# Kernel tuning notes

Measured on AMD Instinct MI355X. Metric: run time of the kernel, lower is better.

Reference implementation:

```python
import jax, jax.numpy as jnp
import numpy as np

# Fixed hyperparameters from init_kwargs
KH, KW = 3, 3
GRID_SIZE = 5
SPLINE_ORDER = 3
GRID_RANGE = (-1.0, 1.0)


def _make_grid():
    # grid buffer: arange(-k, grid_size + k + 1) * h + grid_range[0], shape (G + 2k + 1,) = (12,)
    h = (GRID_RANGE[1] - GRID_RANGE[0]) / GRID_SIZE
    return (jnp.arange(-SPLINE_ORDER, GRID_SIZE + SPLINE_ORDER + 1, dtype=jnp.float32) * h
            + GRID_RANGE[0])


def _unfold(x):
    # torch.nn.Unfold with kernel (3,3), stride 1, pad 0, dilation 1.
    # Returns (N, C*KH*KW) with channel-major ordering (c, i, j), matching torch.
    B, C, H, W = x.shape
    Ho, Wo = H - KH + 1, W - KW + 1
    cols = [x[:, :, i:i + Ho, j:j + Wo] for i in range(KH) for j in range(KW)]
    p = jnp.stack(cols, axis=2)                    # (B, C, KH*KW, Ho, Wo)
    p = p.reshape(B, C * KH * KW, Ho * Wo)         # (B, in_features, L)
    p = p.transpose(0, 2, 1).reshape(-1, C * KH * KW)  # (B*L, in_features)
    return p, Ho, Wo


def _b_splines(x, grid):
    # x: (N, in_features); grid: (G + 2k + 1,) uniform, shared across features.
    # Returns (N, in_features, G + k) B-spline basis via Cox-de Boor recursion.
    x = x[..., None]  # (N, in, 1)
    bases = ((x >= grid[:-1]) & (x < grid[1:])).astype(x.dtype)  # (N, in, G+2k)
    for k in range(1, SPLINE_ORDER + 1):
        left = (x - grid[: -(k + 1)]) / (grid[k:-1] - grid[: -(k + 1)])
        right = (grid[k + 1:] - x) / (grid[k + 1:] - grid[1:-k])
        bases = left * bases[..., :-1] + right * bases[..., 1:]
    return bases  # (N, in, G + k)


def setup_inputs() -> dict:
    key = jax.random.key(0)
    k1, k2, k3, k4 = jax.random.split(key, 4)
    in_features = 32 * KH * KW  # 288
    out_features = 64
    n_coef = GRID_SIZE + SPLINE_ORDER  # 8
    x = jax.random.normal(k1, (16, 32, 64, 64), dtype=jnp.float32)
    base_weight = jax.random.normal(k2, (out_features, in_features), dtype=jnp.float32) * (1.0 / np.sqrt(in_features))
    spline_weight = jax.random.normal(k3, (out_features, in_features, n_coef), dtype=jnp.float32) * 0.1
    spline_scaler = jax.random.normal(k4, (out_features, in_features), dtype=jnp.float32) * (1.0 / np.sqrt(in_features))
    return {"x": x, "base_weight": base_weight, "spline_weight": spline_weight,
            "spline_scaler": spline_scaler}


def reference(x, base_weight, spline_weight, spline_scaler):
    B = x.shape[0]
    out_features = base_weight.shape[0]
    grid = _make_grid()

    patches, Ho, Wo = _unfold(x)                              # (N, in_features)
    N, in_features = patches.shape

    # KANLinear forward
    base_out = jnp.matmul(jax.nn.relu(patches), base_weight.T)  # (N, out)
    bases = _b_splines(patches, grid)                           # (N, in, G+k)
    scaled_w = spline_weight * spline_scaler[..., None]         # (out, in, G+k)
    spline_out = jnp.matmul(bases.reshape(N, -1), scaled_w.reshape(out_features, -1).T)
    out = base_out + spline_out                                 # (N, out)

    out = out.reshape(B, Ho, Wo, out_features).transpose(0, 3, 1, 2)  # (B, C_out, Ho, Wo)
    return out
```

## Files before the change

### kernel.cpp

```cpp
#include <hip/hip_runtime.h>
#include <stdint.h>

typedef _Float16 half8  __attribute__((ext_vector_type(8)));
typedef float    f32x4  __attribute__((ext_vector_type(4)));
typedef uint32_t u32x4  __attribute__((ext_vector_type(4)));

#define FIN  288
#define NOUT 64
#define LPB  3844
#define KSPL 72
#define NBF  20736
#define NBAS (16*64*32*64)
#define NXR  (16*64*64*4)
#define PADS 16

#define SCL  200
#define LDSL (31*SCL + 2*64 + 64 + 8)


__device__ inline half8 bspline8(float xv) {
  float u = fmaf(xv, 2.5f, 5.5f);
  float fi = floorf(u);
  int i = (int)fi;
  float t = u - fi, s = 1.0f - t;
  float t2 = t * t, t3 = t2 * t;
  float s2 = s * s, s3 = s2 * s;
  float w3 = t3 * 0.16666667f;
  float w0 = s3 * 0.16666667f;
  float w1 = fmaf(0.5f, t3, -t2) + 0.66666667f;
  float w2 = fmaf(0.5f, s3, -s2) + 0.66666667f;
  uint32_t u01 = __builtin_bit_cast(uint32_t, __builtin_amdgcn_cvt_pkrtz(w0, w1));
  uint32_t u23 = __builtin_bit_cast(uint32_t, __builtin_amdgcn_cvt_pkrtz(w2, w3));
  uint64_t V = (uint64_t)u01 | ((uint64_t)u23 << 32);
  uint32_t vl = (uint32_t)(V << 16);
  u32x4 fr;
#pragma unroll
  for (int q = 0; q < 4; ++q) {
    int d = i - 2 * q;
    uint32_t rr = (uint32_t)(V >> ((48 - 16 * d) & 63));
    fr[q] = ((uint32_t)d <= 3u) ? rr : ((d == 4) ? vl : 0u);
  }
  return __builtin_bit_cast(half8, fr);
}

__global__ __launch_bounds__(256) void prep_all(const float* __restrict__ x,
                                                const float* __restrict__ bw,
                                                const float* __restrict__ sw,
                                                const float* __restrict__ sc,
                                                half8* __restrict__ ws) {
  int bid = blockIdx.x;
  if (bid < 2048) {
    int t = bid * 256 + threadIdx.x;
    int w4 = t & 15;
    int cperm = (t >> 4) & 31;
    int bh = t >> 9;
    int c = ((cperm & 7) << 2) | (cperm >> 3);
    const float4 v = *(const float4*)(x + (bh >> 6) * 131072 + c * 4096 +
                                      (bh & 63) * 64 + w4 * 4);
    half8* dst = ws + NBF + (size_t)t * 4;
    dst[0] = bspline8(v.x);
    dst[1] = bspline8(v.y);
    dst[2] = bspline8(v.z);
    dst[3] = bspline8(v.w);
  } else if (bid < 3072) {
    int t = (bid - 2048) * 256 + threadIdx.x;
    int quad = t & 3;
    int w = (t >> 2) & 63;
    int bh = t >> 8;
    const float* xp = x + (bh >> 6) * 131072 + (quad * 8) * 4096 + (bh & 63) * 64 + w;
    half8 v;
#pragma unroll
    for (int j = 0; j < 8; ++j) v[j] = (_Float16)fmaxf(xp[j * 4096], 0.0f);
    ws[NBF + NBAS + t] = v;
  } else {
    int t = (bid - 3072) * 256 + threadIdx.x;
    half8 v;
    int dst;
    if (t < NOUT * FIN) {
      int o = t / FIN;
      int f = t - o * FIN;
      float scale = sc[t];
      const float* p = sw + t * 8;
#pragma unroll
      for (int c = 0; c < 8; ++c) v[c] = (_Float16)(p[c] * scale);
      int ch = f / 9;
      int r  = f - ch * 9;
      int ii = r / 3;
      int jj = r - ii * 3;
      int g  = ch >> 2, q = ch & 3;
      int kt = ii * 24 + jj * 8 + g;
      dst = (kt * 4 + (o >> 4)) * 64 + q * 16 + (o & 15);
    } else {
      int t2 = t - NOUT * FIN;
      int lane = t2 & 63;
      int nf = (t2 >> 6) & 3;
      int ktb = t2 >> 8;
      int o = nf * 16 + (lane & 15);
      int q = lane >> 4;
      int i2 = ktb / 3;
      int j2 = ktb - 3 * i2;
#pragma unroll
      for (int c0 = 0; c0 < 8; ++c0)
        v[c0] = (_Float16)bw[o * FIN + 9 * (q * 8 + c0) + 3 * i2 + j2];
      dst = ((KSPL + ktb) * 4 + nf) * 64 + lane;
    }
    ws[dst] = v;
  }
}

__global__ __launch_bounds__(512, 2) void kan_main(
    const half8* __restrict__ ws,
    float* __restrict__ out) {
  __shared__ __align__(16) unsigned char ldsraw[65536];
  half8* lbf0 = (half8*)ldsraw;
  half8* lbf1 = (half8*)(ldsraw + 32768);
  float* red  = (float*)ldsraw;

  const half8* __restrict__ bfrag = ws;
  const half8* __restrict__ bas   = ws + NBF;
  const half8* __restrict__ xr    = ws + NBF + NBAS;

  const int tid = threadIdx.x;
  int bid0 = blockIdx.x;
  int bid = (bid0 & 7) * 32 + (bid0 >> 3);
  const int b  = bid >> 4;
  const int hg = bid & 15;

  const int lane = tid & 63;
  const int wv   = tid >> 6;
  const int g2   = wv >> 2;
  const int rw   = wv & 3;
  const int quad = lane >> 4;
  const int m16  = lane & 15;
  const int ho   = hg * 4 + rw;
  const int hoc  = ho < 61 ? ho : 61;
  const int glo  = g2 * 4;

  f32x4 acc[4][4];
#pragma unroll
  for (int mt = 0; mt < 4; ++mt)
#pragma unroll
    for (int nf = 0; nf < 4; ++nf) acc[mt][nf] = (f32x4){0.f, 0.f, 0.f, 0.f};

  const half8* bb = bas + ((b * 64 + hoc) * 32 + quad * 8) * 64 + m16;

#pragma unroll
  for (int i = 0; i < 4; ++i) {
    int idx = i * 512 + tid;
    lbf0[idx] = bfrag[idx];
  }
  __syncthreads();
  half8* bcur = lbf0;
  half8* balt = lbf1;

  for (int pp = 0; pp < 9; ++pp) {
    half8 stg[4];
    if (pp < 8) {
      const half8* src = bfrag + (pp + 1) * 2048;
#pragma unroll
      for (int i = 0; i < 4; ++i) stg[i] = src[i * 512 + tid];
    }

    int ii = (pp * 11) >> 5;
    int jj = pp - 3 * ii;
    const half8* pA = bb + ii * 2048 + jj;
#pragma unroll
    for (int gg = 0; gg < 4; ++gg) {
      const int g = glo + gg;
      half8 af[4];
#pragma unroll
      for (int mt = 0; mt < 4; ++mt) af[mt] = pA[g * 64 + mt * 16];
#pragma unroll
      for (int nf = 0; nf < 4; ++nf) {
        half8 bf = bcur[g * 256 + nf * 64 + lane];
#pragma unroll
        for (int mt = 0; mt < 4; ++mt)
          acc[mt][nf] = __builtin_amdgcn_mfma_f32_16x16x32_f16(af[mt], bf, acc[mt][nf], 0, 0, 0);
      }
    }

    if (pp < 8) {
#pragma unroll
      for (int i = 0; i < 4; ++i) balt[i * 512 + tid] = stg[i];
    }
    __syncthreads();
    half8* t = bcur; bcur = balt; balt = t;
  }

  const int klo = g2 ? 4 : 0;
  const int khi = g2 ? 9 : 4;
  for (int kb = klo; kb < khi; ++kb) {
    int i2 = (kb * 11) >> 5;
    int j2 = kb - 3 * i2;
    const half8* q = xr + ((b * 64 + hoc + i2) * 64 + m16 + j2) * 4 + quad;
    half8 af[4];
#pragma unroll
    for (int mt = 0; mt < 4; ++mt) af[mt] = q[mt * 64];
    const half8* bfp = bfrag + (KSPL + kb) * 256 + lane;
#pragma unroll
    for (int nf = 0; nf < 4; ++nf) {
      half8 bf = bfp[nf * 64];
#pragma unroll
      for (int mt = 0; mt < 4; ++mt)
        acc[mt][nf] = __builtin_amdgcn_mfma_f32_16x16x32_f16(af[mt], bf, acc[mt][nf], 0, 0, 0);
    }
  }

  if (g2) {
    int base = (rw * 64 + lane) * 64;
#pragma unroll
    for (int mt = 0; mt < 4; ++mt)
#pragma unroll
      for (int nf = 0; nf < 4; ++nf) {
        int pos = ((mt * 4 + nf) + lane) & 15;
        *(f32x4*)&red[base + pos * 4] = acc[mt][nf];
      }
  }
  __syncthreads();

  if (!g2) {
    int base = (rw * 64 + lane) * 64;
#pragma unroll
    for (int mt = 0; mt < 4; ++mt)
#pragma unroll
      for (int nf = 0; nf < 4; ++nf) {
        int pos = ((mt * 4 + nf) + lane) & 15;
        acc[mt][nf] += *(const f32x4*)&red[base + pos * 4];
      }

    if (ho < 62) {
      float* ob = out + b * (NOUT * LPB) + ho * 62;
#pragma unroll
      for (int mt = 0; mt < 4; ++mt) {
#pragma unroll
        for (int rg = 0; rg < 4; ++rg) {
          int wo2 = mt * 16 + quad * 4 + rg;
          if (wo2 < 62) {
#pragma unroll
            for (int nf = 0; nf < 4; ++nf) {
              int o = nf * 16 + m16;
              ob[o * LPB + wo2] = acc[mt][nf][rg];
            }
          }
        }
      }
    }
  }
}

__global__ void prep_bfrag_legacy(const float* __restrict__ bw,
                                  const float* __restrict__ sw,
                                  const float* __restrict__ sc,
                                  half8* __restrict__ bfrag) {
  int t = blockIdx.x * 256 + threadIdx.x;
  half8 v;
  int dst;
  if (t < NOUT * FIN) {
    int o = t / FIN;
    int f = t - o * FIN;
    float scale = sc[t];
    const float* p = sw + t * 8;
#pragma unroll
    for (int c = 0; c < 8; ++c) v[c] = (_Float16)(p[c] * scale);
    int ch = f / 9;
    int r  = f - ch * 9;
    int ii = r / 3;
    int jj = r - ii * 3;
    int g  = ch >> 2, q = ch & 3;
    int kt = ii * 24 + jj * 8 + g;
    dst = (kt * 4 + (o >> 4)) * 64 + q * 16 + (o & 15);
  } else {
    int t2 = t - NOUT * FIN;
    int lane = t2 & 63;
    int nf = (t2 >> 6) & 3;
    int ktb = t2 >> 8;
    int o = nf * 16 + (lane & 15);
    int f0 = ktb * 32 + (lane >> 4) * 8;
    const float* p = bw + o * FIN + f0;
#pragma unroll
    for (int c = 0; c < 8; ++c) v[c] = (_Float16)p[c];
    dst = ((KSPL + ktb) * 4 + nf) * 64 + lane;
  }
  bfrag[dst] = v;
}

__global__ __launch_bounds__(256, 4) void kan_main_legacy(
    const float* __restrict__ x,
    const half8* __restrict__ bfrag,
    float* __restrict__ out) {
  __shared__ float lx[LDSL];
  const int tid = threadIdx.x;
  const int bid = blockIdx.x;
  const int b  = bid / 62;
  const int ho = bid - b * 62;
  const float* xb = x + b * 131072 + ho * 64;
#pragma unroll
  for (int r = 0; r < 6; ++r) {
    int gid = r * 256 + tid;
    int row = gid >> 4;
    int c   = (row * 683) >> 11;
    int ii  = row - c * 3;
    int colv = (gid & 15) * 4;
    const float4 v = *(const float4*)(xb + c * 4096 + ii * 64 + colv);
    *(float4*)(&lx[c * SCL + ii * 64 + colv]) = v;
  }
  __syncthreads();
  const int lane = tid & 63;
  const int wv   = tid >> 6;
  const int quad = lane >> 4;
  const int m16  = lane & 15;
  const int wo   = wv * 16 + m16;
  f32x4 acc[4];
#pragma unroll
  for (int nf = 0; nf < 4; ++nf) acc[nf] = (f32x4){0.f, 0.f, 0.f, 0.f};
  int kt = 0;
#pragma unroll
  for (int ii = 0; ii < 3; ++ii) {
#pragma unroll
    for (int jj = 0; jj < 3; ++jj) {
      const float* lbase = lx + quad * SCL + ii * 64 + wo + jj;
#pragma unroll
      for (int g = 0; g < 8; ++g) {
        float xv = lbase[g * (4 * SCL)];
        half8 af = bspline8(xv);
#pragma unroll
        for (int nf = 0; nf < 4; ++nf) {
          half8 bf = bfrag[(kt * 4 + nf) * 64 + lane];
          acc[nf] = __builtin_amdgcn_mfma_f32_16x16x32_f16(af, bf, acc[nf], 0, 0, 0);
        }
        ++kt;
      }
    }
  }
#pragma unroll
  for (int kb = 0; kb < 9; ++kb) {
    int f0 = kb * 32 + quad * 8;
    half8 a;
#pragma unroll
    for (int j = 0; j < 8; ++j) {
      int f = f0 + j;
      int c = (f * 57) >> 9;
      int r = f - c * 9;
      int i2 = (r * 11) >> 5;
      int j2 = r - i2 * 3;
      a[j] = (_Float16)fmaxf(lx[c * SCL + i2 * 64 + wo + j2], 0.0f);
    }
#pragma unroll
    for (int nf = 0; nf < 4; ++nf) {
      half8 bf = bfrag[((KSPL + kb) * 4 + nf) * 64 + lane];
      acc[nf] = __builtin_amdgcn_mfma_f32_16x16x32_f16(a, bf, acc[nf], 0, 0, 0);
    }
  }
  float* ob = out + b * (NOUT * LPB) + ho * 62;
#pragma unroll
  for (int rg = 0; rg < 4; ++rg) {
    int wo2 = wv * 16 + quad * 4 + rg;
    if (wo2 < 62) {
#pragma unroll
      for (int nf = 0; nf < 4; ++nf) {
        int o = nf * 16 + m16;
        ob[o * LPB + wo2] = acc[nf][rg];
      }
    }
  }
}

extern "C" void kernel_launch(void* const* d_in, const int* in_sizes, int n_in,
                              void* d_out, int out_size, void* d_ws, size_t ws_size,
                              hipStream_t stream) {
  const float* x  = (const float*)d_in[0];
  const float* bw = (const float*)d_in[1];
  const float* sw = (const float*)d_in[2];
  const float* sc = (const float*)d_in[3];
  float* out = (float*)d_out;
  half8* ws = (half8*)d_ws;

  const size_t need = (size_t)(NBF + NBAS + NXR + PADS) * sizeof(half8);
  if (ws_size >= need) {
    prep_all<<<3153, 256, 0, stream>>>(x, bw, sw, sc, ws);
    kan_main<<<256, 512, 0, stream>>>(ws, out);
  } else {
    prep_bfrag_legacy<<<81, 256, 0, stream>>>(bw, sw, sc, ws);
    kan_main_legacy<<<16 * 62, 256, 0, stream>>>(x, ws, out);
  }
}
```

Baseline: 122.0 us.

## Switch main GEMM from 16x16x32 to 32x32x16 MFMA with relaid fragments

Replaces the 16x16x32 f16 MFMA tiles with 32x32x16 MFMA. The prep kernel now writes the basis, relu-input and weight fragments in a layout matching the 32-lane operand pattern, and the accumulator, reduction and output indexing change to match. The aim is fewer MFMA issues and fewer operand loads per FLOP. The risks are longer-latency instructions and different global load patterns for the A fragments.

```diff
diff --git a/kernel.cpp b/kernel.cpp
--- a/kernel.cpp
+++ b/kernel.cpp
@@ -3,15 +3,15 @@
 
 typedef _Float16 half8  __attribute__((ext_vector_type(8)));
 typedef float    f32x4  __attribute__((ext_vector_type(4)));
+typedef float    f32x16 __attribute__((ext_vector_type(16)));
 typedef uint32_t u32x4  __attribute__((ext_vector_type(4)));
 
 #define FIN  288
 #define NOUT 64
 #define LPB  3844
-#define KSPL 72
 #define NBF  20736
-#define NBAS (16*64*32*64)
-#define NXR  (16*64*64*4)
+#define NBAS (16*64*16*64*2)
+#define NXR  (16*64*2*64*2)
 #define PADS 16
 
 #define SCL  200
@@ -51,27 +51,31 @@
   int bid = blockIdx.x;
   if (bid < 2048) {
     int t = bid * 256 + threadIdx.x;
-    int w4 = t & 15;
-    int cperm = (t >> 4) & 31;
-    int bh = t >> 9;
-    int c = ((cperm & 7) << 2) | (cperm >> 3);
+    int w4   = t & 15;
+    int idx  = t >> 4;
+    int half = idx & 1;
+    int u    = (idx >> 1) & 15;
+    int bh   = idx >> 5;
+    int c    = u * 2 + half;
     const float4 v = *(const float4*)(x + (bh >> 6) * 131072 + c * 4096 +
                                       (bh & 63) * 64 + w4 * 4);
-    half8* dst = ws + NBF + (size_t)t * 4;
+    half8* dst = ws + NBF + ((size_t)(bh * 16 + u) * 64 + w4 * 4) * 2 + half;
     dst[0] = bspline8(v.x);
-    dst[1] = bspline8(v.y);
-    dst[2] = bspline8(v.z);
-    dst[3] = bspline8(v.w);
+    dst[2] = bspline8(v.y);
+    dst[4] = bspline8(v.z);
+    dst[6] = bspline8(v.w);
   } else if (bid < 3072) {
     int t = (bid - 2048) * 256 + threadIdx.x;
-    int quad = t & 3;
-    int w = (t >> 2) & 63;
-    int bh = t >> 8;
-    const float* xp = x + (bh >> 6) * 131072 + (quad * 8) * 4096 + (bh & 63) * 64 + w;
+    int half = t & 1;
+    int w    = (t >> 1) & 63;
+    int u    = (t >> 7) & 1;
+    int bh   = t >> 8;
+    const float* xp = x + (bh >> 6) * 131072 + (u * 16 + half * 8) * 4096 +
+                      (bh & 63) * 64 + w;
     half8 v;
 #pragma unroll
     for (int j = 0; j < 8; ++j) v[j] = (_Float16)fmaxf(xp[j * 4096], 0.0f);
-    ws[NBF + NBAS + t] = v;
+    ws[NBF + NBAS + ((size_t)(bh * 2 + u) * 64 + w) * 2 + half] = v;
   } else {
     int t = (bid - 3072) * 256 + threadIdx.x;
     half8 v;
@@ -82,27 +86,27 @@
       float scale = sc[t];
       const float* p = sw + t * 8;
 #pragma unroll
-      for (int c = 0; c < 8; ++c) v[c] = (_Float16)(p[c] * scale);
-      int ch = f / 9;
-      int r  = f - ch * 9;
+      for (int j = 0; j < 8; ++j) v[j] = (_Float16)(p[j] * scale);
+      int c  = f / 9;
+      int r  = f - c * 9;
       int ii = r / 3;
       int jj = r - ii * 3;
-      int g  = ch >> 2, q = ch & 3;
-      int kt = ii * 24 + jj * 8 + g;
-      dst = (kt * 4 + (o >> 4)) * 64 + q * 16 + (o & 15);
+      int pp = ii * 3 + jj;
+      int u  = c >> 1, half = c & 1;
+      int nf = o >> 5, col = o & 31;
+      dst = pp * 2048 + u * 128 + nf * 64 + half * 32 + col;
     } else {
       int t2 = t - NOUT * FIN;
       int lane = t2 & 63;
-      int nf = (t2 >> 6) & 3;
-      int ktb = t2 >> 8;
-      int o = nf * 16 + (lane & 15);
-      int q = lane >> 4;
-      int i2 = ktb / 3;
-      int j2 = ktb - 3 * i2;
-#pragma unroll
-      for (int c0 = 0; c0 < 8; ++c0)
-        v[c0] = (_Float16)bw[o * FIN + 9 * (q * 8 + c0) + 3 * i2 + j2];
-      dst = ((KSPL + ktb) * 4 + nf) * 64 + lane;
+      int nf   = (t2 >> 6) & 1;
+      int u    = (t2 >> 7) & 1;
+      int pos  = t2 >> 8;
+      int half = lane >> 5, col = lane & 31;
+      int o = nf * 32 + col;
+#pragma unroll
+      for (int j = 0; j < 8; ++j)
+        v[j] = (_Float16)bw[o * FIN + 9 * (u * 16 + half * 8 + j) + pos];
+      dst = NOUT * FIN + t2;
     }
     ws[dst] = v;
   }
@@ -130,19 +134,22 @@
   const int wv   = tid >> 6;
   const int g2   = wv >> 2;
   const int rw   = wv & 3;
-  const int quad = lane >> 4;
-  const int m16  = lane & 15;
+  const int l31  = lane & 31;
+  const int lhi  = lane >> 5;
+  const int laneoff = l31 * 2 + lhi;
   const int ho   = hg * 4 + rw;
   const int hoc  = ho < 61 ? ho : 61;
-  const int glo  = g2 * 4;
-
-  f32x4 acc[4][4];
-#pragma unroll
-  for (int mt = 0; mt < 4; ++mt)
-#pragma unroll
-    for (int nf = 0; nf < 4; ++nf) acc[mt][nf] = (f32x4){0.f, 0.f, 0.f, 0.f};
-
-  const half8* bb = bas + ((b * 64 + hoc) * 32 + quad * 8) * 64 + m16;
+  const int ulo  = g2 * 8;
+
+  f32x16 acc[2][2];
+#pragma unroll
+  for (int mt = 0; mt < 2; ++mt)
+#pragma unroll
+    for (int nf = 0; nf < 2; ++nf)
+#pragma unroll
+      for (int e = 0; e < 16; ++e) acc[mt][nf][e] = 0.f;
+
+  const half8* bbS = bas + (size_t)(b * 64 + hoc) * 2048 + laneoff;
 
 #pragma unroll
   for (int i = 0; i < 4; ++i) {
@@ -163,19 +170,17 @@
 
     int ii = (pp * 11) >> 5;
     int jj = pp - 3 * ii;
-    const half8* pA = bb + ii * 2048 + jj;
-#pragma unroll
-    for (int gg = 0; gg < 4; ++gg) {
-      const int g = glo + gg;
-      half8 af[4];
-#pragma unroll
-      for (int mt = 0; mt < 4; ++mt) af[mt] = pA[g * 64 + mt * 16];
-#pragma unroll
-      for (int nf = 0; nf < 4; ++nf) {
-        half8 bf = bcur[g * 256 + nf * 64 + lane];
-#pragma unroll
-        for (int mt = 0; mt < 4; ++mt)
-          acc[mt][nf] = __builtin_amdgcn_mfma_f32_16x16x32_f16(af[mt], bf, acc[mt][nf], 0, 0, 0);
+    const half8* pAf = bbS + ii * 2048 + jj * 2;
+#pragma unroll
+    for (int uu = 0; uu < 8; ++uu) {
+      const int u = ulo + uu;
+      half8 af0 = pAf[u * 128];
+      half8 af1 = pAf[u * 128 + 64];
+#pragma unroll
+      for (int nf = 0; nf < 2; ++nf) {
+        half8 bf = bcur[u * 128 + nf * 64 + lane];
+        acc[0][nf] = __builtin_amdgcn_mfma_f32_32x32x16_f16(af0, bf, acc[0][nf], 0, 0, 0);
+        acc[1][nf] = __builtin_amdgcn_mfma_f32_32x32x16_f16(af1, bf, acc[1][nf], 0, 0, 0);
       }
     }
 
@@ -187,59 +192,66 @@
     half8* t = bcur; bcur = balt; balt = t;
   }
 
-  const int klo = g2 ? 4 : 0;
-  const int khi = g2 ? 9 : 4;
-  for (int kb = klo; kb < khi; ++kb) {
-    int i2 = (kb * 11) >> 5;
-    int j2 = kb - 3 * i2;
-    const half8* q = xr + ((b * 64 + hoc + i2) * 64 + m16 + j2) * 4 + quad;
-    half8 af[4];
-#pragma unroll
-    for (int mt = 0; mt < 4; ++mt) af[mt] = q[mt * 64];
-    const half8* bfp = bfrag + (KSPL + kb) * 256 + lane;
-#pragma unroll
-    for (int nf = 0; nf < 4; ++nf) {
+  for (int pos = 0; pos < 9; ++pos) {
+    int i2 = (pos * 11) >> 5;
+    int j2 = pos - 3 * i2;
+    const half8* pAf = xr + (size_t)((b * 64 + hoc + i2) * 2 + g2) * 128 +
+                       j2 * 2 + laneoff;
+    half8 af0 = pAf[0];
+    half8 af1 = pAf[64];
+    const half8* bfp = bfrag + NOUT * FIN + (pos * 2 + g2) * 128 + lane;
+#pragma unroll
+    for (int nf = 0; nf < 2; ++nf) {
       half8 bf = bfp[nf * 64];
-#pragma unroll
-      for (int mt = 0; mt < 4; ++mt)
-        acc[mt][nf] = __builtin_amdgcn_mfma_f32_16x16x32_f16(af[mt], bf, acc[mt][nf], 0, 0, 0);
+      acc[0][nf] = __builtin_amdgcn_mfma_f32_32x32x16_f16(af0, bf, acc[0][nf], 0, 0, 0);
+      acc[1][nf] = __builtin_amdgcn_mfma_f32_32x32x16_f16(af1, bf, acc[1][nf], 0, 0, 0);
     }
   }
 
   if (g2) {
     int base = (rw * 64 + lane) * 64;
 #pragma unroll
-    for (int mt = 0; mt < 4; ++mt)
-#pragma unroll
-      for (int nf = 0; nf < 4; ++nf) {
-        int pos = ((mt * 4 + nf) + lane) & 15;
-        *(f32x4*)&red[base + pos * 4] = acc[mt][nf];
-      }
+    for (int mt = 0; mt < 2; ++mt)
+#pragma unroll
+      for (int nf = 0; nf < 2; ++nf)
+#pragma unroll
+        for (int q4 = 0; q4 < 4; ++q4) {
+          int pos = ((mt * 8 + nf * 4 + q4) + lane) & 15;
+          f32x4 ch = {acc[mt][nf][q4 * 4], acc[mt][nf][q4 * 4 + 1],
+                      acc[mt][nf][q4 * 4 + 2], acc[mt][nf][q4 * 4 + 3]};
+          *(f32x4*)&red[base + pos * 4] = ch;
+        }
   }
   __syncthreads();
 
   if (!g2) {
     int base = (rw * 64 + lane) * 64;
 #pragma unroll
-    for (int mt = 0; mt < 4; ++mt)
-#pragma unroll
-      for (int nf = 0; nf < 4; ++nf) {
-        int pos = ((mt * 4 + nf) + lane) & 15;
-        acc[mt][nf] += *(const f32x4*)&red[base + pos * 4];
-      }
+    for (int mt = 0; mt < 2; ++mt)
+#pragma unroll
+      for (int nf = 0; nf < 2; ++nf)
+#pragma unroll
+        for (int q4 = 0; q4 < 4; ++q4) {
+          int pos = ((mt * 8 + nf * 4 + q4) + lane) & 15;
+          f32x4 ch = *(const f32x4*)&red[base + pos * 4];
+          acc[mt][nf][q4 * 4]     += ch[0];
+          acc[mt][nf][q4 * 4 + 1] += ch[1];
+          acc[mt][nf][q4 * 4 + 2] += ch[2];
+          acc[mt][nf][q4 * 4 + 3] += ch[3];
+        }
 
     if (ho < 62) {
       float* ob = out + b * (NOUT * LPB) + ho * 62;
 #pragma unroll
-      for (int mt = 0; mt < 4; ++mt) {
-#pragma unroll
-        for (int rg = 0; rg < 4; ++rg) {
-          int wo2 = mt * 16 + quad * 4 + rg;
+      for (int mt = 0; mt < 2; ++mt) {
+#pragma unroll
+        for (int reg = 0; reg < 16; ++reg) {
+          int wo2 = mt * 32 + (reg & 3) + 8 * (reg >> 2) + 4 * lhi;
           if (wo2 < 62) {
 #pragma unroll
-            for (int nf = 0; nf < 4; ++nf) {
-              int o = nf * 16 + m16;
-              ob[o * LPB + wo2] = acc[mt][nf][rg];
+            for (int nf = 0; nf < 2; ++nf) {
+              int o = nf * 32 + l31;
+              ob[o * LPB + wo2] = acc[mt][nf][reg];
             }
           }
         }
@@ -248,6 +260,7 @@
   }
 }
 
+#define KSPL 72
 __global__ void prep_bfrag_legacy(const float* __restrict__ bw,
                                   const float* __restrict__ sw,
                                   const float* __restrict__ sc,
```

Measured after the change: 119.9 us. About the same (-1.7%).
